# Performance work log

Measured on AMD Instinct MI355X. Metric: run time of the kernel, lower is better.

The kernel has to match this reference:

```python
import jax, jax.numpy as jnp
import numpy as np

N, NT, NX, H, M, DH, DIN = 16, 128, 128, 64, 12, 128, 128


def _spectral_conv(h, w1, w2, m):
    # h: [B,C,Ht,Wt]; w1,w2: complex [C,C,m,m]
    B, C, Ht, Wt = h.shape
    hft = jnp.fft.rfft2(h)  # [B,C,Ht,Wt//2+1] complex
    top = jnp.einsum('bixy,ioxy->boxy', hft[:, :, :m, :m], w1)
    bot = jnp.einsum('bixy,ioxy->boxy', hft[:, :, -m:, :m], w2)
    out_ft = jnp.zeros((B, w1.shape[1], Ht, Wt // 2 + 1), dtype=hft.dtype)
    out_ft = out_ft.at[:, :, :m, :m].set(top).at[:, :, -m:, :m].set(bot)
    return jnp.fft.irfft2(out_ft, s=(Ht, Wt))


def setup_inputs() -> dict:
    key = jax.random.key(0)
    ks = jax.random.split(key, 16)
    scale = 1.0 / (H * H)
    inp = {
        't': jax.random.uniform(ks[0], (NT,), jnp.float32),
        'x': jax.random.uniform(ks[1], (NX,), jnp.float32),
        'u0': jax.random.normal(ks[2], (N, DIN), jnp.float32),
        'fc0_w': jax.random.normal(ks[3], (H, DIN + 2), jnp.float32) / np.sqrt(DIN + 2),
        'fc0_b': jnp.zeros((H,), jnp.float32),
        'sc_w1_re': scale * jax.random.uniform(ks[4], (4, H, H, M, M), jnp.float32),
        'sc_w1_im': scale * jax.random.uniform(ks[5], (4, H, H, M, M), jnp.float32),
        'sc_w2_re': scale * jax.random.uniform(ks[6], (4, H, H, M, M), jnp.float32),
        'sc_w2_im': scale * jax.random.uniform(ks[7], (4, H, H, M, M), jnp.float32),
        'w_conv': jax.random.normal(ks[8], (4, H, H), jnp.float32) / np.sqrt(H),
        'b_conv': jnp.zeros((4, H), jnp.float32),
        'fc1_w': jax.random.normal(ks[9], (DH, H), jnp.float32) / np.sqrt(H),
        'fc1_b': jnp.zeros((DH,), jnp.float32),
        'fc2_w': jax.random.normal(ks[10], (1, DH), jnp.float32) / np.sqrt(DH),
        'fc2_b': jnp.zeros((1,), jnp.float32),
    }
    return inp


def reference(t, x, u0, fc0_w, fc0_b, sc_w1_re, sc_w1_im, sc_w2_re, sc_w2_im,
              w_conv, b_conv, fc1_w, fc1_b, fc2_w, fc2_b):
    nt, nx = t.shape[0], x.shape[0]
    n, din = u0.shape
    gelu = lambda v: jax.nn.gelu(v, approximate=False)  # torch F.gelu default (erf)
    # grid features, column order (x, t, u0) per torch hstack([query, aug_u0])
    xg = jnp.broadcast_to(x[None, None, :, None], (n, nt, nx, 1))
    tg = jnp.broadcast_to(t[None, :, None, None], (n, nt, nx, 1))
    ug = jnp.broadcast_to(u0[:, None, None, :], (n, nt, nx, din))
    h = jnp.concatenate([xg, tg, ug], axis=-1) @ fc0_w.T + fc0_b  # [N,Nt,Nx,H]
    h = jnp.transpose(h, (0, 3, 1, 2))  # [N,H,Nt,Nx]
    m = sc_w1_re.shape[-1]
    for i in range(4):
        w1 = sc_w1_re[i] + 1j * sc_w1_im[i]
        w2 = sc_w2_re[i] + 1j * sc_w2_im[i]
        x1 = _spectral_conv(h, w1, w2, m)
        x2 = jnp.einsum('bchw,oc->bohw', h, w_conv[i]) + b_conv[i][None, :, None, None]
        h = x1 + x2
        if i < 3:
            h = gelu(h)
    h = jnp.transpose(h, (0, 2, 3, 1))  # [N,Nt,Nx,H]
    h = gelu(h @ fc1_w.T + fc1_b)
    out = (h @ fc2_w.T + fc2_b)[..., 0]  # squeeze -> [N,Nt,Nx]
    return out
```

## Files before the change

kernel.cpp:

```cpp
#include <hip/hip_runtime.h>
#include <math.h>


typedef __attribute__((ext_vector_type(8))) short short8;
typedef __attribute__((ext_vector_type(4))) float f32x4;

__device__ inline unsigned short bf16rn(float v) {
    unsigned int b = __float_as_uint(v);
    return (unsigned short)((b + 0x7FFFu + ((b >> 16) & 1u)) >> 16);
}
__device__ inline void split2(float v, unsigned short& h, unsigned short& l) {
    h = bf16rn(v);
    float hf = __uint_as_float((unsigned int)h << 16);
    l = bf16rn(v - hf);
}
__device__ inline short8 ld8(const unsigned short* p) {
    return *reinterpret_cast<const short8*>(p);
}
__device__ inline float gelu_erf(float v) {
    return 0.5f * v * (1.0f + erff(v * 0.70710678118654752f));
}
#define MFMA3(accv, aH, aL, bH, bL) \
    accv = __builtin_amdgcn_mfma_f32_16x16x32_bf16(aH, bH, accv, 0, 0, 0); \
    accv = __builtin_amdgcn_mfma_f32_16x16x32_bf16(aH, bL, accv, 0, 0, 0); \
    accv = __builtin_amdgcn_mfma_f32_16x16x32_bf16(aL, bH, accv, 0, 0, 0);

#define STEPC 0.049087385212340519350f

__global__ __launch_bounds__(256) void k_tables2(unsigned short* TfH, unsigned short* TfL,
                                                 unsigned short* TiXH, unsigned short* TiXL,
                                                 unsigned short* TDH, unsigned short* TDL,
                                                 unsigned short* TIH, unsigned short* TIL) {
    int tid = threadIdx.x;
    unsigned short h, l;
    for (int i = tid; i < 32 * 128; i += 256) {
        int row = i >> 7, x = i & 127;
        float v = 0.f;
        if (row < 24) {
            int kx = row >> 1;
            float th = ((kx * x) & 127) * STEPC;
            v = (row & 1) ? -sinf(th) : cosf(th);
        }
        split2(v, h, l); TfH[i] = h; TfL[i] = l;
    }
    for (int i = tid; i < 128 * 32; i += 256) {
        int x = i >> 5, col = i & 31;
        float v = 0.f;
        if (col < 24) {
            int kx = col >> 1;
            float th = ((kx * x) & 127) * STEPC;
            float w = (kx == 0 ? 1.0f : 2.0f) / 16384.0f;
            v = (col & 1) ? -w * sinf(th) : w * cosf(th);
        }
        split2(v, h, l); TiXH[i] = h; TiXL[i] = l;
    }
    for (int i = tid; i < 48 * 256; i += 256) {
        int row = i >> 8, k = i & 255;
        int kt = row >> 1;
        int f = (kt < 12) ? kt : (kt + 104);
        int t = k & 127;
        float th = ((f * t) & 127) * STEPC;
        float c = cosf(th), s = sinf(th);
        float v;
        if (k < 128) v = (row & 1) ? -s : c;
        else         v = (row & 1) ?  c : s;
        split2(v, h, l); TDH[i] = h; TDL[i] = l;
    }
    for (int i = tid; i < 128 * 64; i += 256) {
        int t = i >> 6, col = i & 63;
        float v = 0.f;
        if (col < 48) {
            int kt = col >> 1;
            int f = (kt < 12) ? kt : (kt + 104);
            float th = ((f * t) & 127) * STEPC;
            v = (col & 1) ? -sinf(th) : cosf(th);
        }
        split2(v, h, l); TIH[i] = h; TIL[i] = l;
    }
}

__global__ void k_spec(const float* __restrict__ xs, const float* __restrict__ ts,
                       float2* __restrict__ Sx, float2* __restrict__ St) {
    int tid = threadIdx.x;
    if (tid < 12) {
        float re = 0.f, im = 0.f;
        for (int x = 0; x < 128; ++x) {
            float th = ((tid * x) & 127) * STEPC;
            re += xs[x] * cosf(th); im -= xs[x] * sinf(th);
        }
        Sx[tid] = make_float2(re, im);
    } else if (tid >= 32 && tid < 56) {
        int kt = tid - 32;
        int f = (kt < 12) ? kt : (kt + 104);
        float re = 0.f, im = 0.f;
        for (int t = 0; t < 128; ++t) {
            float th = ((f * t) & 127) * STEPC;
            re += ts[t] * cosf(th); im -= ts[t] * sinf(th);
        }
        St[kt] = make_float2(re, im);
    }
}

__global__ __launch_bounds__(256) void k_wprep(const float* __restrict__ wconv, const float* __restrict__ fc1w,
                                               unsigned short* WH, unsigned short* WL,
                                               unsigned short* F1H, unsigned short* F1L) {
    int i = blockIdx.x * 256 + threadIdx.x;
    if (i < 16384) split2(wconv[i], WH[i], WL[i]);
    if (i < 8192)  split2(fc1w[i], F1H[i], F1L[i]);
}

__global__ void k_u(const float* __restrict__ u0, const float* __restrict__ w,
                    const float* __restrict__ bias, float* __restrict__ U) {
    int b = blockIdx.x, c = threadIdx.x;
    float acc = bias[c];
    const float* wr = w + c * 130 + 2;
    const float* ur = u0 + b * 128;
    for (int d = 0; d < 128; ++d) acc += ur[d] * wr[d];
    U[b * 64 + c] = acc;
}

__global__ __launch_bounds__(256) void k_fc0t(const float* __restrict__ xs, const float* __restrict__ ts,
                                              const float* __restrict__ fc0_w, const float* __restrict__ U,
                                              unsigned short* __restrict__ hTH, unsigned short* __restrict__ hTL) {
    __shared__ float w0c[64], basec[64];
    int bid = blockIdx.x, tid = threadIdx.x;
    int t = bid & 127, b = bid >> 7;
    if (tid < 64) {
        w0c[tid] = fc0_w[tid * 130];
        basec[tid] = ts[t] * fc0_w[tid * 130 + 1] + U[b * 64 + tid];
    }
    __syncthreads();
    int x = tid >> 1, c0 = (tid & 1) * 32;
    float xv = xs[x];
    unsigned int ph[16], pl[16];
#pragma unroll
    for (int j = 0; j < 32; j += 2) {
        unsigned short h0, l0, h1, l1;
        split2(xv * w0c[c0 + j] + basec[c0 + j], h0, l0);
        split2(xv * w0c[c0 + j + 1] + basec[c0 + j + 1], h1, l1);
        ph[j >> 1] = (unsigned)h0 | ((unsigned)h1 << 16);
        pl[j >> 1] = (unsigned)l0 | ((unsigned)l1 << 16);
    }
    size_t rb = ((size_t)((b * 128 + t) * 128 + x)) * 64 + c0;
    uint4* dh = reinterpret_cast<uint4*>(&hTH[rb]);
    uint4* dl = reinterpret_cast<uint4*>(&hTL[rb]);
#pragma unroll
    for (int q = 0; q < 4; ++q) {
        dh[q] = make_uint4(ph[4 * q], ph[4 * q + 1], ph[4 * q + 2], ph[4 * q + 3]);
        dl[q] = make_uint4(pl[4 * q], pl[4 * q + 1], pl[4 * q + 2], pl[4 * q + 3]);
    }
}

__global__ __launch_bounds__(256) void k_hm0(const float* __restrict__ fc0_w, const float* __restrict__ U,
                                             const float2* __restrict__ Sx, const float2* __restrict__ St,
                                             float2* __restrict__ Hm) {
    __shared__ float w0s[64], w1s[64];
    int mode = blockIdx.x, tid = threadIdx.x;
    int kt = mode / 12, kx = mode - kt * 12;
    if (tid < 64) { w0s[tid] = fc0_w[tid * 130]; w1s[tid] = fc0_w[tid * 130 + 1]; }
    __syncthreads();
    float2 sx = Sx[kx], st = St[kt];
    for (int i = tid; i < 1024; i += 256) {
        int b = i >> 6, c = i & 63;
        float re = 0.f, im = 0.f;
        if (kt == 0) { re += 128.f * w0s[c] * sx.x; im += 128.f * w0s[c] * sx.y; }
        if (kx == 0) { re += 128.f * w1s[c] * st.x; im += 128.f * w1s[c] * st.y; }
        if (kt == 0 && kx == 0) re += 16384.f * U[b * 64 + c];
        Hm[((size_t)mode * 16 + b) * 64 + c] = make_float2(re, im);
    }
}

__global__ __launch_bounds__(256) void k_wt(const float* __restrict__ w1re, const float* __restrict__ w1im,
                                            const float* __restrict__ w2re, const float* __restrict__ w2im,
                                            float2* __restrict__ Wt) {
    __shared__ float ldsre[32 * 145];
    __shared__ float ldsim[32 * 145];
    int bid = blockIdx.x, tid = threadIdx.x;
    int c = bid & 63, tbl = (bid >> 6) & 1, l = bid >> 7;
    const float* re = (tbl ? w2re : w1re) + (size_t)((l * 64 + c) * 64) * 144;
    const float* im = (tbl ? w2im : w1im) + (size_t)((l * 64 + c) * 64) * 144;
    int moff = tbl * 144;
    for (int half = 0; half < 2; ++half) {
        __syncthreads();
        for (int i = tid; i < 32 * 144; i += 256) {
            int o = i / 144, m = i - o * 144;
            ldsre[o * 145 + m] = re[(half * 32 + o) * 144 + m];
            ldsim[o * 145 + m] = im[(half * 32 + o) * 144 + m];
        }
        __syncthreads();
        for (int i = tid; i < 32 * 144; i += 256) {
            int mode = i >> 5, o = i & 31;
            Wt[((size_t)(l * 288 + moff + mode) * 64 + c) * 64 + half * 32 + o] =
                make_float2(ldsre[o * 145 + mode], ldsim[o * 145 + mode]);
        }
    }
}

__global__ __launch_bounds__(256) void k_dftt2(const unsigned short* __restrict__ A2H, const unsigned short* __restrict__ A2L,
                                               const unsigned short* __restrict__ TDH, const unsigned short* __restrict__ TDL,
                                               float2* __restrict__ Hm) {
    int bid = blockIdx.x, tid = threadIdx.x;
    int b = bid / 12, kx = bid - b * 12;
    int w = tid >> 6, lane = tid & 63, ln = lane & 15, lg = lane >> 4;
    f32x4 acc[3];
#pragma unroll
    for (int m = 0; m < 3; ++m) acc[m] = (f32x4){0.f, 0.f, 0.f, 0.f};
    size_t reb = (size_t)(b * 24 + 2 * kx) * 64 * 128;
    size_t imb = (size_t)(b * 24 + 2 * kx + 1) * 64 * 128;
    int c = w * 16 + ln;
#pragma unroll
    for (int ks = 0; ks < 8; ++ks) {
        int k = ks * 32 + lg * 8;
        size_t boff = (ks < 4) ? (reb + (size_t)c * 128 + k) : (imb + (size_t)c * 128 + (k - 128));
        short8 bH = ld8(A2H + boff);
        short8 bL = ld8(A2L + boff);
#pragma unroll
        for (int m = 0; m < 3; ++m) {
            int aoff = (m * 16 + ln) * 256 + ks * 32 + lg * 8;
            short8 aH = ld8(TDH + aoff);
            short8 aL = ld8(TDL + aoff);
            MFMA3(acc[m], aH, aL, bH, bL);
        }
    }
    float* Hf = (float*)Hm;
#pragma unroll
    for (int m = 0; m < 3; ++m)
#pragma unroll
        for (int r = 0; r < 4; ++r) {
            int row = m * 16 + lg * 4 + r;
            int kt = row >> 1, p = row & 1;
            int mode = kt * 12 + kx;
            Hf[(((size_t)mode * 16 + b) * 64 + c) * 2 + p] = acc[m][r];
        }
}

__global__ __launch_bounds__(256) void k_mix(const float2* __restrict__ Hm, const float2* __restrict__ WtL,
                                             float2* __restrict__ Om) {
    __shared__ float2 hl[8 * 64];
    int bid = blockIdx.x, tid = threadIdx.x;
    int mode = bid >> 1, bh = bid & 1;
    const float2* hsrc = Hm + ((size_t)mode * 16 + bh * 8) * 64;
    for (int i = tid; i < 512; i += 256) hl[i] = hsrc[i];
    __syncthreads();
    int o = tid & 63, bg = tid >> 6;
    const float2* wp = WtL + (size_t)mode * 4096 + o;
    const float2* h0 = hl + (bg * 2) * 64;
    const float2* h1 = hl + (bg * 2 + 1) * 64;
    float a0r = 0.f, a0i = 0.f, a1r = 0.f, a1i = 0.f;
#pragma unroll 4
    for (int c = 0; c < 64; ++c) {
        float2 wv = wp[c * 64];
        float2 a0 = h0[c], a1 = h1[c];
        a0r += a0.x * wv.x - a0.y * wv.y;
        a0i += a0.x * wv.y + a0.y * wv.x;
        a1r += a1.x * wv.x - a1.y * wv.y;
        a1i += a1.x * wv.y + a1.y * wv.x;
    }
    int b0 = bh * 8 + bg * 2;
    Om[((size_t)(b0)*64 + o) * 288 + mode]       = make_float2(a0r, a0i);
    Om[((size_t)(b0 + 1) * 64 + o) * 288 + mode] = make_float2(a1r, a1i);
}

__global__ __launch_bounds__(256) void k_mix_raw(const float2* __restrict__ Hm,
                                                 const float* __restrict__ w1re, const float* __restrict__ w1im,
                                                 const float* __restrict__ w2re, const float* __restrict__ w2im,
                                                 float2* __restrict__ Om) {
    __shared__ float2 hl[8 * 64];
    int bid = blockIdx.x, tid = threadIdx.x;
    int mode = bid >> 1, bh = bid & 1;
    const float2* hsrc = Hm + ((size_t)mode * 16 + bh * 8) * 64;
    for (int i = tid; i < 512; i += 256) hl[i] = hsrc[i];
    __syncthreads();
    int kti = mode / 12, kx = mode - kti * 12;
    const float* re; const float* im; int ktw;
    if (kti < 12) { re = w1re; im = w1im; ktw = kti; }
    else          { re = w2re; im = w2im; ktw = kti - 12; }
    int off = ktw * 12 + kx;
    int o = tid & 63, bg = tid >> 6;
    const float2* h0 = hl + (bg * 2) * 64;
    const float2* h1 = hl + (bg * 2 + 1) * 64;
    float a0r = 0.f, a0i = 0.f, a1r = 0.f, a1i = 0.f;
    for (int c = 0; c < 64; ++c) {
        size_t widx = (size_t)(c * 64 + o) * 144 + off;
        float wr = re[widx], wi = im[widx];
        float2 a0 = h0[c], a1 = h1[c];
        a0r += a0.x * wr - a0.y * wi;
        a0i += a0.x * wi + a0.y * wr;
        a1r += a1.x * wr - a1.y * wi;
        a1i += a1.x * wi + a1.y * wr;
    }
    int b0 = bh * 8 + bg * 2;
    Om[((size_t)(b0)*64 + o) * 288 + mode]       = make_float2(a0r, a0i);
    Om[((size_t)(b0 + 1) * 64 + o) * 288 + mode] = make_float2(a1r, a1i);
}

__global__ __launch_bounds__(256) void k_idftt2(const float2* __restrict__ Om,
                                                const unsigned short* __restrict__ TIH, const unsigned short* __restrict__ TIL,
                                                unsigned short* __restrict__ BvH, unsigned short* __restrict__ BvL) {
    __shared__ unsigned short OmH[32][72], OmL[32][72];
    int bo = blockIdx.x, tid = threadIdx.x;
    unsigned int* zh = (unsigned int*)&OmH[0][0];
    unsigned int* zl = (unsigned int*)&OmL[0][0];
    for (int i = tid; i < 1152; i += 256) { zh[i] = 0u; zl[i] = 0u; }
    __syncthreads();
    const float2* src = Om + (size_t)bo * 288;
    for (int i = tid; i < 288; i += 256) {
        int kt = i / 12, kx = i - kt * 12;
        float2 o = src[i];
        unsigned short h, l;
        split2(o.x, h, l);  OmH[2 * kx][2 * kt] = h;     OmL[2 * kx][2 * kt] = l;
        split2(o.y, h, l);  OmH[2 * kx][2 * kt + 1] = h; OmL[2 * kx][2 * kt + 1] = l;
                            OmH[2 * kx + 1][2 * kt] = h; OmL[2 * kx + 1][2 * kt] = l;
        split2(-o.x, h, l); OmH[2 * kx + 1][2 * kt + 1] = h; OmL[2 * kx + 1][2 * kt + 1] = l;
    }
    __syncthreads();
    int w = tid >> 6, lane = tid & 63, ln = lane & 15, lg = lane >> 4;
    f32x4 acc[2][2];
#pragma unroll
    for (int mi = 0; mi < 2; ++mi)
#pragma unroll
        for (int nt = 0; nt < 2; ++nt) acc[mi][nt] = (f32x4){0.f, 0.f, 0.f, 0.f};
#pragma unroll
    for (int ks = 0; ks < 2; ++ks) {
        short8 bH[2], bL[2];
#pragma unroll
        for (int nt = 0; nt < 2; ++nt) {
            int boff = (nt * 16 + ln) * 72 + ks * 32 + lg * 8;
            bH[nt] = ld8(&OmH[0][0] + boff);
            bL[nt] = ld8(&OmL[0][0] + boff);
        }
#pragma unroll
        for (int mi = 0; mi < 2; ++mi) {
            int mt = w * 2 + mi;
            int aoff = (mt * 16 + ln) * 64 + ks * 32 + lg * 8;
            short8 aH = ld8(TIH + aoff);
            short8 aL = ld8(TIL + aoff);
#pragma unroll
            for (int nt = 0; nt < 2; ++nt) { MFMA3(acc[mi][nt], aH, aL, bH[nt], bL[nt]); }
        }
    }
#pragma unroll
    for (int mi = 0; mi < 2; ++mi)
#pragma unroll
        for (int nt = 0; nt < 2; ++nt)
#pragma unroll
            for (int r = 0; r < 4; ++r) {
                int trow = (w * 2 + mi) * 16 + lg * 4 + r;
                int col = nt * 16 + ln;
                unsigned short h, l;
                split2(acc[mi][nt][r], h, l);
                size_t p = ((size_t)bo * 128 + trow) * 32 + col;
                BvH[p] = h; BvL[p] = l;
            }
}

template <int DOGELU, int FUSE>
__global__ __launch_bounds__(256) void k_conv3(unsigned short* __restrict__ hTH, unsigned short* __restrict__ hTL,
                                               const unsigned short* __restrict__ WH, const unsigned short* __restrict__ WL,
                                               const unsigned short* __restrict__ BvH, const unsigned short* __restrict__ BvL,
                                               const unsigned short* __restrict__ TiXH, const unsigned short* __restrict__ TiXL,
                                               const unsigned short* __restrict__ TfH, const unsigned short* __restrict__ TfL,
                                               unsigned short* __restrict__ A2H, unsigned short* __restrict__ A2L,
                                               const float* __restrict__ bconv) {
    __shared__ float hsf[64][132];
    int bid = blockIdx.x, tid = threadIdx.x;
    int t = bid & 127, b = bid >> 7;
    int w = tid >> 6, lane = tid & 63, ln = lane & 15, lg = lane >> 4;
    size_t btbase = (size_t)(b * 128 + t) * 128 * 64;
    f32x4 acc[8];
#pragma unroll
    for (int nx = 0; nx < 8; ++nx) acc[nx] = (f32x4){0.f, 0.f, 0.f, 0.f};
#pragma unroll
    for (int kt = 0; kt < 2; ++kt) {
        int aoff = (w * 16 + ln) * 64 + kt * 32 + lg * 8;
        short8 aH = ld8(WH + aoff);
        short8 aL = ld8(WL + aoff);
#pragma unroll
        for (int nx = 0; nx < 8; ++nx) {
            size_t boff = btbase + (size_t)(nx * 16 + ln) * 64 + kt * 32 + lg * 8;
            short8 bH = ld8(hTH + boff);
            short8 bL = ld8(hTL + boff);
            MFMA3(acc[nx], aH, aL, bH, bL);
        }
    }
    {
        size_t aoff = ((size_t)(b * 64 + w * 16 + ln) * 128 + t) * 32 + lg * 8;
        short8 aH = ld8(BvH + aoff);
        short8 aL = ld8(BvL + aoff);
#pragma unroll
        for (int nx = 0; nx < 8; ++nx) {
            int boff = (nx * 16 + ln) * 32 + lg * 8;
            short8 bH = ld8(TiXH + boff);
            short8 bL = ld8(TiXL + boff);
            MFMA3(acc[nx], aH, aL, bH, bL);
        }
    }
    __syncthreads();
    int o0 = w * 16 + lg * 4;
    float bc0 = bconv[o0], bc1 = bconv[o0 + 1], bc2 = bconv[o0 + 2], bc3 = bconv[o0 + 3];
#pragma unroll
    for (int nx = 0; nx < 8; ++nx) {
        int x = nx * 16 + ln;
        float v0 = acc[nx][0] + bc0;
        float v1 = acc[nx][1] + bc1;
        float v2 = acc[nx][2] + bc2;
        float v3 = acc[nx][3] + bc3;
        if (DOGELU) { v0 = gelu_erf(v0); v1 = gelu_erf(v1); v2 = gelu_erf(v2); v3 = gelu_erf(v3); }
        unsigned short hh[4], ll[4];
        split2(v0, hh[0], ll[0]); split2(v1, hh[1], ll[1]);
        split2(v2, hh[2], ll[2]); split2(v3, hh[3], ll[3]);
        size_t trow = btbase + (size_t)x * 64 + o0;
        *reinterpret_cast<uint2*>(&hTH[trow]) =
            make_uint2((unsigned)hh[0] | ((unsigned)hh[1] << 16), (unsigned)hh[2] | ((unsigned)hh[3] << 16));
        *reinterpret_cast<uint2*>(&hTL[trow]) =
            make_uint2((unsigned)ll[0] | ((unsigned)ll[1] << 16), (unsigned)ll[2] | ((unsigned)ll[3] << 16));
        if (FUSE) {
            hsf[o0 + 0][x] = v0; hsf[o0 + 1][x] = v1;
            hsf[o0 + 2][x] = v2; hsf[o0 + 3][x] = v3;
        }
    }
    if (FUSE) {
        __syncthreads();
        int mw = w & 1, ng = (w >> 1) * 2;
        f32x4 acc2[2];
        acc2[0] = (f32x4){0.f, 0.f, 0.f, 0.f};
        acc2[1] = (f32x4){0.f, 0.f, 0.f, 0.f};
#pragma unroll
        for (int kt = 0; kt < 4; ++kt) {
            int aoff = (mw * 16 + ln) * 128 + kt * 32 + lg * 8;
            short8 aH = ld8(TfH + aoff);
            short8 aL = ld8(TfL + aoff);
#pragma unroll
            for (int j = 0; j < 2; ++j) {
                int c = (ng + j) * 16 + ln;
                float4 f0 = *reinterpret_cast<const float4*>(&hsf[c][kt * 32 + lg * 8]);
                float4 f1 = *reinterpret_cast<const float4*>(&hsf[c][kt * 32 + lg * 8 + 4]);
                short8 bH, bL;
                unsigned short h, l;
                split2(f0.x, h, l); bH[0] = (short)h; bL[0] = (short)l;
                split2(f0.y, h, l); bH[1] = (short)h; bL[1] = (short)l;
                split2(f0.z, h, l); bH[2] = (short)h; bL[2] = (short)l;
                split2(f0.w, h, l); bH[3] = (short)h; bL[3] = (short)l;
                split2(f1.x, h, l); bH[4] = (short)h; bL[4] = (short)l;
                split2(f1.y, h, l); bH[5] = (short)h; bL[5] = (short)l;
                split2(f1.z, h, l); bH[6] = (short)h; bL[6] = (short)l;
                split2(f1.w, h, l); bH[7] = (short)h; bL[7] = (short)l;
                MFMA3(acc2[j], aH, aL, bH, bL);
            }
        }
#pragma unroll
        for (int j = 0; j < 2; ++j) {
            int c = (ng + j) * 16 + ln;
#pragma unroll
            for (int r = 0; r < 4; ++r) {
                int col = mw * 16 + lg * 4 + r;
                if (col < 24) {
                    unsigned short h, l;
                    split2(acc2[j][r], h, l);
                    size_t addr = ((size_t)(b * 24 + col) * 64 + c) * 128 + t;
                    A2H[addr] = h; A2L[addr] = l;
                }
            }
        }
    }
}

__global__ __launch_bounds__(256) void k_head2(const unsigned short* __restrict__ hTH, const unsigned short* __restrict__ hTL,
                                               const unsigned short* __restrict__ F1H, const unsigned short* __restrict__ F1L,
                                               const float* __restrict__ b1, const float* __restrict__ w2,
                                               const float* __restrict__ b2, float* __restrict__ out) {
    __shared__ float red[16][66];
    int bid = blockIdx.x, tid = threadIdx.x;
    int xh = bid & 1, t = (bid >> 1) & 127, b = bid >> 8;
    int w = tid >> 6, lane = tid & 63, ln = lane & 15, lg = lane >> 4;
    f32x4 acc[2][4];
#pragma unroll
    for (int s = 0; s < 2; ++s)
#pragma unroll
        for (int nx = 0; nx < 4; ++nx) acc[s][nx] = (f32x4){0.f, 0.f, 0.f, 0.f};
    size_t btbase = ((size_t)(b * 128 + t) * 128 + xh * 64) * 64;
#pragma unroll
    for (int kt = 0; kt < 2; ++kt) {
        short8 bH[4], bL[4];
#pragma unroll
        for (int nx = 0; nx < 4; ++nx) {
            size_t boff = btbase + (size_t)(nx * 16 + ln) * 64 + kt * 32 + lg * 8;
            bH[nx] = ld8(hTH + boff);
            bL[nx] = ld8(hTL + boff);
        }
#pragma unroll
        for (int s = 0; s < 2; ++s) {
            int aoff = ((w * 2 + s) * 16 + ln) * 64 + kt * 32 + lg * 8;
            short8 aH = ld8(F1H + aoff);
            short8 aL = ld8(F1L + aoff);
#pragma unroll
            for (int nx = 0; nx < 4; ++nx) { MFMA3(acc[s][nx], aH, aL, bH[nx], bL[nx]); }
        }
    }
    float p[4] = {0.f, 0.f, 0.f, 0.f};
#pragma unroll
    for (int s = 0; s < 2; ++s)
#pragma unroll
        for (int r = 0; r < 4; ++r) {
            int d = (w * 2 + s) * 16 + lg * 4 + r;
            float bb = b1[d], wk = w2[d];
#pragma unroll
            for (int nx = 0; nx < 4; ++nx) {
                float v = acc[s][nx][r] + bb;
                p[nx] += gelu_erf(v) * wk;
            }
        }
#pragma unroll
    for (int nx = 0; nx < 4; ++nx) red[w * 4 + lg][nx * 16 + ln] = p[nx];
    __syncthreads();
    if (tid < 64) {
        float s = 0.f;
#pragma unroll
        for (int g = 0; g < 16; ++g) s += red[g][tid];
        out[((size_t)b * 128 + t) * 128 + xh * 64 + tid] = s + b2[0];
    }
}

extern "C" void kernel_launch(void* const* d_in, const int* in_sizes, int n_in,
                              void* d_out, int out_size, void* d_ws, size_t ws_size,
                              hipStream_t stream) {
    const float* ts    = (const float*)d_in[0];
    const float* xs    = (const float*)d_in[1];
    const float* u0    = (const float*)d_in[2];
    const float* fc0_w = (const float*)d_in[3];
    const float* fc0_b = (const float*)d_in[4];
    const float* w1re  = (const float*)d_in[5];
    const float* w1im  = (const float*)d_in[6];
    const float* w2re  = (const float*)d_in[7];
    const float* w2im  = (const float*)d_in[8];
    const float* wconv = (const float*)d_in[9];
    const float* bconv = (const float*)d_in[10];
    const float* fc1w  = (const float*)d_in[11];
    const float* fc1b  = (const float*)d_in[12];
    const float* fc2w  = (const float*)d_in[13];
    const float* fc2b  = (const float*)d_in[14];
    float* out = (float*)d_out;

    char* ws = (char*)d_ws;
    size_t off = 0;
    auto alloc = [&](size_t bytes) -> char* {
        char* p = ws + off;
        off = (off + bytes + 255) & ~(size_t)255;
        return p;
    };
    unsigned short* hTH = (unsigned short*)alloc(33554432);
    unsigned short* hTL = (unsigned short*)alloc(33554432);
    unsigned short* A2H = (unsigned short*)alloc(6291456);
    unsigned short* A2L = (unsigned short*)alloc(6291456);
    float2* Hm = (float2*)alloc(2359296);
    float2* Om = (float2*)alloc(2359296);
    unsigned short* BvH = (unsigned short*)alloc(8388608);
    unsigned short* BvL = (unsigned short*)alloc(8388608);
    float* U   = (float*)alloc(4096);
    float2* Sx = (float2*)alloc(256);
    float2* St = (float2*)alloc(256);
    unsigned short* TfH  = (unsigned short*)alloc(8192);
    unsigned short* TfL  = (unsigned short*)alloc(8192);
    unsigned short* TiXH = (unsigned short*)alloc(8192);
    unsigned short* TiXL = (unsigned short*)alloc(8192);
    unsigned short* TDH  = (unsigned short*)alloc(24576);
    unsigned short* TDL  = (unsigned short*)alloc(24576);
    unsigned short* TIH  = (unsigned short*)alloc(16384);
    unsigned short* TIL  = (unsigned short*)alloc(16384);
    unsigned short* WH   = (unsigned short*)alloc(32768);
    unsigned short* WL   = (unsigned short*)alloc(32768);
    unsigned short* F1H  = (unsigned short*)alloc(16384);
    unsigned short* F1L  = (unsigned short*)alloc(16384);
    size_t base_need = off;
    if (ws_size < base_need) return;
    float2* Wt = (float2*)alloc(37748736);
    bool use_wt = (ws_size >= off);

    k_tables2<<<1, 256, 0, stream>>>(TfH, TfL, TiXH, TiXL, TDH, TDL, TIH, TIL);
    k_spec<<<1, 64, 0, stream>>>(xs, ts, Sx, St);
    k_u<<<16, 64, 0, stream>>>(u0, fc0_w, fc0_b, U);
    k_wprep<<<64, 256, 0, stream>>>(wconv, fc1w, WH, WL, F1H, F1L);
    k_fc0t<<<2048, 256, 0, stream>>>(xs, ts, fc0_w, U, hTH, hTL);
    k_hm0<<<288, 256, 0, stream>>>(fc0_w, U, Sx, St, Hm);
    if (use_wt)
        k_wt<<<512, 256, 0, stream>>>(w1re, w1im, w2re, w2im, Wt);

    for (int l = 0; l < 4; ++l) {
        if (l > 0)
            k_dftt2<<<192, 256, 0, stream>>>(A2H, A2L, TDH, TDL, Hm);
        if (use_wt)
            k_mix<<<576, 256, 0, stream>>>(Hm, Wt + (size_t)l * 288 * 4096, Om);
        else
            k_mix_raw<<<576, 256, 0, stream>>>(Hm, w1re + (size_t)l * 589824, w1im + (size_t)l * 589824,
                                               w2re + (size_t)l * 589824, w2im + (size_t)l * 589824, Om);
        k_idftt2<<<1024, 256, 0, stream>>>(Om, TIH, TIL, BvH, BvL);
        if (l < 3)
            k_conv3<1, 1><<<2048, 256, 0, stream>>>(hTH, hTL, WH + l * 4096, WL + l * 4096,
                                                    BvH, BvL, TiXH, TiXL, TfH, TfL, A2H, A2L, bconv + l * 64);
        else
            k_conv3<0, 0><<<2048, 256, 0, stream>>>(hTH, hTL, WH + l * 4096, WL + l * 4096,
                                                    BvH, BvL, TiXH, TiXL, TfH, TfL, A2H, A2L, bconv + l * 64);
    }
    k_head2<<<4096, 256, 0, stream>>>(hTH, hTL, F1H, F1L, fc1b, fc2w, fc2b, out);
}
```

Baseline: 724.6 us.

## Fuse fc0 lifting into layer-0 conv, fuse last conv with head, relayout A2

Removes the k_fc0t kernel, which materialised the lifted hidden state, by noting that layer 0's pointwise conv of an affine function of (x, t, U) is itself affine. Precomputed W·fc0 columns and W·U+bias are applied in the layer-0 epilogue, so the first hT read and MFMA are skipped. The final conv layer is fused with the fc1/gelu/fc2 head through shared memory, avoiding a full hT write and re-read. The A2 intermediate is also changed to a t-major, channel-contiguous layout written with vectorised stores through LDS, and k_dftt2 transposes it in LDS. The cost is more LDS traffic and synchronisation, and higher register pressure in the fused head kernel.

Result: faster. 610.7 us (-15.7%).

```diff
diff --git a/kernel.cpp b/kernel.cpp
--- a/kernel.cpp
+++ b/kernel.cpp
@@ -54,16 +54,17 @@
         }
         split2(v, h, l); TiXH[i] = h; TiXL[i] = l;
     }
-    for (int i = tid; i < 48 * 256; i += 256) {
-        int row = i >> 8, k = i & 255;
+    for (int i = tid; i < 2 * 48 * 128; i += 256) {
+        int q = i >> 12;
+        int rem = i & 6143;
+        int row = rem >> 7, t = rem & 127;
         int kt = row >> 1;
         int f = (kt < 12) ? kt : (kt + 104);
-        int t = k & 127;
         float th = ((f * t) & 127) * STEPC;
         float c = cosf(th), s = sinf(th);
         float v;
-        if (k < 128) v = (row & 1) ? -s : c;
-        else         v = (row & 1) ?  c : s;
+        if (q == 0) v = (row & 1) ? -s : c;
+        else        v = (row & 1) ?  c : s;
         split2(v, h, l); TDH[i] = h; TDL[i] = l;
     }
     for (int i = tid; i < 128 * 64; i += 256) {
@@ -101,14 +102,6 @@
     }
 }
 
-__global__ __launch_bounds__(256) void k_wprep(const float* __restrict__ wconv, const float* __restrict__ fc1w,
-                                               unsigned short* WH, unsigned short* WL,
-                                               unsigned short* F1H, unsigned short* F1L) {
-    int i = blockIdx.x * 256 + threadIdx.x;
-    if (i < 16384) split2(wconv[i], WH[i], WL[i]);
-    if (i < 8192)  split2(fc1w[i], F1H[i], F1L[i]);
-}
-
 __global__ void k_u(const float* __restrict__ u0, const float* __restrict__ w,
                     const float* __restrict__ bias, float* __restrict__ U) {
     int b = blockIdx.x, c = threadIdx.x;
@@ -119,35 +112,30 @@
     U[b * 64 + c] = acc;
 }
 
-__global__ __launch_bounds__(256) void k_fc0t(const float* __restrict__ xs, const float* __restrict__ ts,
-                                              const float* __restrict__ fc0_w, const float* __restrict__ U,
-                                              unsigned short* __restrict__ hTH, unsigned short* __restrict__ hTL) {
-    __shared__ float w0c[64], basec[64];
-    int bid = blockIdx.x, tid = threadIdx.x;
-    int t = bid & 127, b = bid >> 7;
-    if (tid < 64) {
-        w0c[tid] = fc0_w[tid * 130];
-        basec[tid] = ts[t] * fc0_w[tid * 130 + 1] + U[b * 64 + tid];
-    }
-    __syncthreads();
-    int x = tid >> 1, c0 = (tid & 1) * 32;
-    float xv = xs[x];
-    unsigned int ph[16], pl[16];
-#pragma unroll
-    for (int j = 0; j < 32; j += 2) {
-        unsigned short h0, l0, h1, l1;
-        split2(xv * w0c[c0 + j] + basec[c0 + j], h0, l0);
-        split2(xv * w0c[c0 + j + 1] + basec[c0 + j + 1], h1, l1);
-        ph[j >> 1] = (unsigned)h0 | ((unsigned)h1 << 16);
-        pl[j >> 1] = (unsigned)l0 | ((unsigned)l1 << 16);
-    }
-    size_t rb = ((size_t)((b * 128 + t) * 128 + x)) * 64 + c0;
-    uint4* dh = reinterpret_cast<uint4*>(&hTH[rb]);
-    uint4* dl = reinterpret_cast<uint4*>(&hTL[rb]);
-#pragma unroll
-    for (int q = 0; q < 4; ++q) {
-        dh[q] = make_uint4(ph[4 * q], ph[4 * q + 1], ph[4 * q + 2], ph[4 * q + 3]);
-        dl[q] = make_uint4(pl[4 * q], pl[4 * q + 1], pl[4 * q + 2], pl[4 * q + 3]);
+__global__ __launch_bounds__(256) void k_wprep(const float* __restrict__ wconv, const float* __restrict__ fc1w,
+                                               unsigned short* WH, unsigned short* WL,
+                                               unsigned short* F1H, unsigned short* F1L) {
+    int i = blockIdx.x * 256 + threadIdx.x;
+    if (i < 16384) split2(wconv[i], WH[i], WL[i]);
+    if (i < 8192)  split2(fc1w[i], F1H[i], F1L[i]);
+}
+
+__global__ void k_cw(const float* __restrict__ wconv, const float* __restrict__ bconv,
+                     const float* __restrict__ fc0_w, const float* __restrict__ U,
+                     float* __restrict__ Ww0, float* __restrict__ Ww1, float* __restrict__ WU) {
+    int b = blockIdx.x, o = threadIdx.x;
+    const float* wr = wconv + o * 64;
+    float au = bconv[o];
+    const float* ur = U + b * 64;
+    for (int c = 0; c < 64; ++c) au += wr[c] * ur[c];
+    WU[b * 64 + o] = au;
+    if (b == 0) {
+        float a0 = 0.f, a1 = 0.f;
+        for (int c = 0; c < 64; ++c) {
+            a0 += wr[c] * fc0_w[c * 130];
+            a1 += wr[c] * fc0_w[c * 130 + 1];
+        }
+        Ww0[o] = a0; Ww1[o] = a1;
     }
 }
 
@@ -199,38 +187,54 @@
 __global__ __launch_bounds__(256) void k_dftt2(const unsigned short* __restrict__ A2H, const unsigned short* __restrict__ A2L,
                                                const unsigned short* __restrict__ TDH, const unsigned short* __restrict__ TDL,
                                                float2* __restrict__ Hm) {
+    __shared__ unsigned short sH[64][136], sL[64][136];
     int bid = blockIdx.x, tid = threadIdx.x;
     int b = bid / 12, kx = bid - b * 12;
     int w = tid >> 6, lane = tid & 63, ln = lane & 15, lg = lane >> 4;
     f32x4 acc[3];
 #pragma unroll
     for (int m = 0; m < 3; ++m) acc[m] = (f32x4){0.f, 0.f, 0.f, 0.f};
-    size_t reb = (size_t)(b * 24 + 2 * kx) * 64 * 128;
-    size_t imb = (size_t)(b * 24 + 2 * kx + 1) * 64 * 128;
+#pragma unroll
+    for (int q = 0; q < 2; ++q) {
+        if (q) __syncthreads();
+        int col = 2 * kx + q;
+        const unsigned short* srcH = A2H + (size_t)(b * 24 + col) * 128 * 64;
+        const unsigned short* srcL = A2L + (size_t)(b * 24 + col) * 128 * 64;
+        for (int i = tid; i < 1024; i += 256) {
+            int t = i >> 3, c0 = (i & 7) * 8;
+            uint4 vh = *reinterpret_cast<const uint4*>(srcH + t * 64 + c0);
+            uint4 vl = *reinterpret_cast<const uint4*>(srcL + t * 64 + c0);
+            const unsigned short* ph = (const unsigned short*)&vh;
+            const unsigned short* pl = (const unsigned short*)&vl;
+#pragma unroll
+            for (int j = 0; j < 8; ++j) {
+                sH[c0 + j][t] = ph[j];
+                sL[c0 + j][t] = pl[j];
+            }
+        }
+        __syncthreads();
+#pragma unroll
+        for (int ks = 0; ks < 4; ++ks) {
+            short8 bH = ld8(&sH[w * 16 + ln][ks * 32 + lg * 8]);
+            short8 bL = ld8(&sL[w * 16 + ln][ks * 32 + lg * 8]);
+#pragma unroll
+            for (int m = 0; m < 3; ++m) {
+                int aoff = (q * 48 + m * 16 + ln) * 128 + ks * 32 + lg * 8;
+                short8 aH = ld8(TDH + aoff);
+                short8 aL = ld8(TDL + aoff);
+                MFMA3(acc[m], aH, aL, bH, bL);
+            }
+        }
+    }
+    float* Hf = (float*)Hm;
     int c = w * 16 + ln;
-#pragma unroll
-    for (int ks = 0; ks < 8; ++ks) {
-        int k = ks * 32 + lg * 8;
-        size_t boff = (ks < 4) ? (reb + (size_t)c * 128 + k) : (imb + (size_t)c * 128 + (k - 128));
-        short8 bH = ld8(A2H + boff);
-        short8 bL = ld8(A2L + boff);
-#pragma unroll
-        for (int m = 0; m < 3; ++m) {
-            int aoff = (m * 16 + ln) * 256 + ks * 32 + lg * 8;
-            short8 aH = ld8(TDH + aoff);
-            short8 aL = ld8(TDL + aoff);
-            MFMA3(acc[m], aH, aL, bH, bL);
-        }
-    }
-    float* Hf = (float*)Hm;
 #pragma unroll
     for (int m = 0; m < 3; ++m)
 #pragma unroll
         for (int r = 0; r < 4; ++r) {
             int row = m * 16 + lg * 4 + r;
-            int kt = row >> 1, p = row & 1;
-            int mode = kt * 12 + kx;
-            Hf[(((size_t)mode * 16 + b) * 64 + c) * 2 + p] = acc[m][r];
+            int kt = row >> 1, pp = row & 1;
+            Hf[(((size_t)(kt * 12 + kx) * 16 + b) * 64 + c) * 2 + pp] = acc[m][r];
         }
 }
 
@@ -331,8 +335,7 @@
         }
 #pragma unroll
         for (int mi = 0; mi < 2; ++mi) {
-            int mt = w * 2 + mi;
-            int aoff = (mt * 16 + ln) * 64 + ks * 32 + lg * 8;
+            int aoff = ((w * 2 + mi) * 16 + ln) * 64 + ks * 32 + lg * 8;
             short8 aH = ld8(TIH + aoff);
             short8 aL = ld8(TIL + aoff);
 #pragma unroll
@@ -354,14 +357,17 @@
             }
 }
 
-template <int DOGELU, int FUSE>
-__global__ __launch_bounds__(256) void k_conv3(unsigned short* __restrict__ hTH, unsigned short* __restrict__ hTL,
-                                               const unsigned short* __restrict__ WH, const unsigned short* __restrict__ WL,
-                                               const unsigned short* __restrict__ BvH, const unsigned short* __restrict__ BvL,
-                                               const unsigned short* __restrict__ TiXH, const unsigned short* __restrict__ TiXL,
-                                               const unsigned short* __restrict__ TfH, const unsigned short* __restrict__ TfL,
-                                               unsigned short* __restrict__ A2H, unsigned short* __restrict__ A2L,
-                                               const float* __restrict__ bconv) {
+template <int AFFINE>
+__global__ __launch_bounds__(256) void k_conv_mid(unsigned short* __restrict__ hTH, unsigned short* __restrict__ hTL,
+                                                  const unsigned short* __restrict__ WH, const unsigned short* __restrict__ WL,
+                                                  const unsigned short* __restrict__ BvH, const unsigned short* __restrict__ BvL,
+                                                  const unsigned short* __restrict__ TiXH, const unsigned short* __restrict__ TiXL,
+                                                  const unsigned short* __restrict__ TfH, const unsigned short* __restrict__ TfL,
+                                                  unsigned short* __restrict__ A2H, unsigned short* __restrict__ A2L,
+                                                  const float* __restrict__ bconv,
+                                                  const float* __restrict__ xs, const float* __restrict__ ts,
+                                                  const float* __restrict__ Ww0, const float* __restrict__ Ww1,
+                                                  const float* __restrict__ WU) {
     __shared__ float hsf[64][132];
     int bid = blockIdx.x, tid = threadIdx.x;
     int t = bid & 127, b = bid >> 7;
@@ -370,17 +376,19 @@
     f32x4 acc[8];
 #pragma unroll
     for (int nx = 0; nx < 8; ++nx) acc[nx] = (f32x4){0.f, 0.f, 0.f, 0.f};
-#pragma unroll
-    for (int kt = 0; kt < 2; ++kt) {
-        int aoff = (w * 16 + ln) * 64 + kt * 32 + lg * 8;
-        short8 aH = ld8(WH + aoff);
-        short8 aL = ld8(WL + aoff);
-#pragma unroll
-        for (int nx = 0; nx < 8; ++nx) {
-            size_t boff = btbase + (size_t)(nx * 16 + ln) * 64 + kt * 32 + lg * 8;
-            short8 bH = ld8(hTH + boff);
-            short8 bL = ld8(hTL + boff);
-            MFMA3(acc[nx], aH, aL, bH, bL);
+    if (!AFFINE) {
+#pragma unroll
+        for (int kt = 0; kt < 2; ++kt) {
+            int aoff = (w * 16 + ln) * 64 + kt * 32 + lg * 8;
+            short8 aH = ld8(WH + aoff);
+            short8 aL = ld8(WL + aoff);
+#pragma unroll
+            for (int nx = 0; nx < 8; ++nx) {
+                size_t boff = btbase + (size_t)(nx * 16 + ln) * 64 + kt * 32 + lg * 8;
+                short8 bH = ld8(hTH + boff);
+                short8 bL = ld8(hTL + boff);
+                MFMA3(acc[nx], aH, aL, bH, bL);
+            }
         }
     }
     {
@@ -397,15 +405,28 @@
     }
     __syncthreads();
     int o0 = w * 16 + lg * 4;
-    float bc0 = bconv[o0], bc1 = bconv[o0 + 1], bc2 = bconv[o0 + 2], bc3 = bconv[o0 + 3];
+    float ad0, ad1, ad2, ad3, w00 = 0.f, w01 = 0.f, w02 = 0.f, w03 = 0.f;
+    float w10 = 0.f, w11 = 0.f, w12 = 0.f, w13 = 0.f, tsv = 0.f;
+    if (AFFINE) {
+        const float* wu = WU + b * 64 + o0;
+        ad0 = wu[0]; ad1 = wu[1]; ad2 = wu[2]; ad3 = wu[3];
+        w00 = Ww0[o0]; w01 = Ww0[o0 + 1]; w02 = Ww0[o0 + 2]; w03 = Ww0[o0 + 3];
+        tsv = ts[t];
+        w10 = Ww1[o0] * tsv; w11 = Ww1[o0 + 1] * tsv; w12 = Ww1[o0 + 2] * tsv; w13 = Ww1[o0 + 3] * tsv;
+        ad0 += w10; ad1 += w11; ad2 += w12; ad3 += w13;
+    } else {
+        ad0 = bconv[o0]; ad1 = bconv[o0 + 1]; ad2 = bconv[o0 + 2]; ad3 = bconv[o0 + 3];
+    }
 #pragma unroll
     for (int nx = 0; nx < 8; ++nx) {
         int x = nx * 16 + ln;
-        float v0 = acc[nx][0] + bc0;
-        float v1 = acc[nx][1] + bc1;
-        float v2 = acc[nx][2] + bc2;
-        float v3 = acc[nx][3] + bc3;
-        if (DOGELU) { v0 = gelu_erf(v0); v1 = gelu_erf(v1); v2 = gelu_erf(v2); v3 = gelu_erf(v3); }
+        float xv = AFFINE ? xs[x] : 0.f;
+        float v0 = acc[nx][0] + ad0;
+        float v1 = acc[nx][1] + ad1;
+        float v2 = acc[nx][2] + ad2;
+        float v3 = acc[nx][3] + ad3;
+        if (AFFINE) { v0 += xv * w00; v1 += xv * w01; v2 += xv * w02; v3 += xv * w03; }
+        v0 = gelu_erf(v0); v1 = gelu_erf(v1); v2 = gelu_erf(v2); v3 = gelu_erf(v3);
         unsigned short hh[4], ll[4];
         split2(v0, hh[0], ll[0]); split2(v1, hh[1], ll[1]);
         split2(v2, hh[2], ll[2]); split2(v3, hh[3], ll[3]);
@@ -414,110 +435,170 @@
             make_uint2((unsigned)hh[0] | ((unsigned)hh[1] << 16), (unsigned)hh[2] | ((unsigned)hh[3] << 16));
         *reinterpret_cast<uint2*>(&hTL[trow]) =
             make_uint2((unsigned)ll[0] | ((unsigned)ll[1] << 16), (unsigned)ll[2] | ((unsigned)ll[3] << 16));
-        if (FUSE) {
-            hsf[o0 + 0][x] = v0; hsf[o0 + 1][x] = v1;
-            hsf[o0 + 2][x] = v2; hsf[o0 + 3][x] = v3;
-        }
-    }
-    if (FUSE) {
-        __syncthreads();
-        int mw = w & 1, ng = (w >> 1) * 2;
-        f32x4 acc2[2];
-        acc2[0] = (f32x4){0.f, 0.f, 0.f, 0.f};
-        acc2[1] = (f32x4){0.f, 0.f, 0.f, 0.f};
-#pragma unroll
-        for (int kt = 0; kt < 4; ++kt) {
-            int aoff = (mw * 16 + ln) * 128 + kt * 32 + lg * 8;
-            short8 aH = ld8(TfH + aoff);
-            short8 aL = ld8(TfL + aoff);
-#pragma unroll
-            for (int j = 0; j < 2; ++j) {
-                int c = (ng + j) * 16 + ln;
-                float4 f0 = *reinterpret_cast<const float4*>(&hsf[c][kt * 32 + lg * 8]);
-                float4 f1 = *reinterpret_cast<const float4*>(&hsf[c][kt * 32 + lg * 8 + 4]);
-                short8 bH, bL;
-                unsigned short h, l;
-                split2(f0.x, h, l); bH[0] = (short)h; bL[0] = (short)l;
-                split2(f0.y, h, l); bH[1] = (short)h; bL[1] = (short)l;
-                split2(f0.z, h, l); bH[2] = (short)h; bL[2] = (short)l;
-                split2(f0.w, h, l); bH[3] = (short)h; bL[3] = (short)l;
-                split2(f1.x, h, l); bH[4] = (short)h; bL[4] = (short)l;
-                split2(f1.y, h, l); bH[5] = (short)h; bL[5] = (short)l;
-                split2(f1.z, h, l); bH[6] = (short)h; bL[6] = (short)l;
-                split2(f1.w, h, l); bH[7] = (short)h; bL[7] = (short)l;
-                MFMA3(acc2[j], aH, aL, bH, bL);
-            }
-        }
+        hsf[o0 + 0][x] = v0; hsf[o0 + 1][x] = v1;
+        hsf[o0 + 2][x] = v2; hsf[o0 + 3][x] = v3;
+    }
+    __syncthreads();
+    int mw = w & 1, ng = (w >> 1) * 2;
+    f32x4 acc2[2];
+    acc2[0] = (f32x4){0.f, 0.f, 0.f, 0.f};
+    acc2[1] = (f32x4){0.f, 0.f, 0.f, 0.f};
+#pragma unroll
+    for (int kt = 0; kt < 4; ++kt) {
+        int aoff = (mw * 16 + ln) * 128 + kt * 32 + lg * 8;
+        short8 aH = ld8(TfH + aoff);
+        short8 aL = ld8(TfL + aoff);
 #pragma unroll
         for (int j = 0; j < 2; ++j) {
             int c = (ng + j) * 16 + ln;
-#pragma unroll
-            for (int r = 0; r < 4; ++r) {
-                int col = mw * 16 + lg * 4 + r;
-                if (col < 24) {
-                    unsigned short h, l;
-                    split2(acc2[j][r], h, l);
-                    size_t addr = ((size_t)(b * 24 + col) * 64 + c) * 128 + t;
-                    A2H[addr] = h; A2L[addr] = l;
-                }
+            float4 f0 = *reinterpret_cast<const float4*>(&hsf[c][kt * 32 + lg * 8]);
+            float4 f1 = *reinterpret_cast<const float4*>(&hsf[c][kt * 32 + lg * 8 + 4]);
+            short8 bH, bL;
+            unsigned short h, l;
+            split2(f0.x, h, l); bH[0] = (short)h; bL[0] = (short)l;
+            split2(f0.y, h, l); bH[1] = (short)h; bL[1] = (short)l;
+            split2(f0.z, h, l); bH[2] = (short)h; bL[2] = (short)l;
+            split2(f0.w, h, l); bH[3] = (short)h; bL[3] = (short)l;
+            split2(f1.x, h, l); bH[4] = (short)h; bL[4] = (short)l;
+            split2(f1.y, h, l); bH[5] = (short)h; bL[5] = (short)l;
+            split2(f1.z, h, l); bH[6] = (short)h; bL[6] = (short)l;
+            split2(f1.w, h, l); bH[7] = (short)h; bL[7] = (short)l;
+            MFMA3(acc2[j], aH, aL, bH, bL);
+        }
+    }
+    __syncthreads();
+    float* A2s = &hsf[0][0];
+#pragma unroll
+    for (int j = 0; j < 2; ++j) {
+        int c = (ng + j) * 16 + ln;
+#pragma unroll
+        for (int r = 0; r < 4; ++r) {
+            int col = mw * 16 + lg * 4 + r;
+            A2s[col * 68 + c] = acc2[j][r];
+        }
+    }
+    __syncthreads();
+    {
+        int col = tid >> 3;
+        if (col < 24) {
+            int c0 = (tid & 7) * 8;
+            unsigned short hh[8], ll[8];
+#pragma unroll
+            for (int j = 0; j < 8; ++j) split2(A2s[col * 68 + c0 + j], hh[j], ll[j]);
+            size_t p = ((size_t)(b * 24 + col) * 128 + t) * 64 + c0;
+            *reinterpret_cast<uint4*>(&A2H[p]) = make_uint4(
+                (unsigned)hh[0] | ((unsigned)hh[1] << 16), (unsigned)hh[2] | ((unsigned)hh[3] << 16),
+                (unsigned)hh[4] | ((unsigned)hh[5] << 16), (unsigned)hh[6] | ((unsigned)hh[7] << 16));
+            *reinterpret_cast<uint4*>(&A2L[p]) = make_uint4(
+                (unsigned)ll[0] | ((unsigned)ll[1] << 16), (unsigned)ll[2] | ((unsigned)ll[3] << 16),
+                (unsigned)ll[4] | ((unsigned)ll[5] << 16), (unsigned)ll[6] | ((unsigned)ll[7] << 16));
+        }
+    }
+}
+
+__global__ __launch_bounds__(256) void k_conv_head(const unsigned short* __restrict__ hTH, const unsigned short* __restrict__ hTL,
+                                                   const unsigned short* __restrict__ WH, const unsigned short* __restrict__ WL,
+                                                   const unsigned short* __restrict__ BvH, const unsigned short* __restrict__ BvL,
+                                                   const unsigned short* __restrict__ TiXH, const unsigned short* __restrict__ TiXL,
+                                                   const float* __restrict__ bconv,
+                                                   const unsigned short* __restrict__ F1H, const unsigned short* __restrict__ F1L,
+                                                   const float* __restrict__ b1, const float* __restrict__ w2,
+                                                   const float* __restrict__ b2, float* __restrict__ out) {
+    __shared__ float hsf[64][132];
+    int bid = blockIdx.x, tid = threadIdx.x;
+    int t = bid & 127, b = bid >> 7;
+    int w = tid >> 6, lane = tid & 63, ln = lane & 15, lg = lane >> 4;
+    size_t btbase = (size_t)(b * 128 + t) * 128 * 64;
+    f32x4 acc[8];
+#pragma unroll
+    for (int nx = 0; nx < 8; ++nx) acc[nx] = (f32x4){0.f, 0.f, 0.f, 0.f};
+#pragma unroll
+    for (int kt = 0; kt < 2; ++kt) {
+        int aoff = (w * 16 + ln) * 64 + kt * 32 + lg * 8;
+        short8 aH = ld8(WH + aoff);
+        short8 aL = ld8(WL + aoff);
+#pragma unroll
+        for (int nx = 0; nx < 8; ++nx) {
+            size_t boff = btbase + (size_t)(nx * 16 + ln) * 64 + kt * 32 + lg * 8;
+            short8 bH = ld8(hTH + boff);
+            short8 bL = ld8(hTL + boff);
+            MFMA3(acc[nx], aH, aL, bH, bL);
+        }
+    }
+    {
+        size_t aoff = ((size_t)(b * 64 + w * 16 + ln) * 128 + t) * 32 + lg * 8;
+        short8 aH = ld8(BvH + aoff);
+        short8 aL = ld8(BvL + aoff);
+#pragma unroll
+        for (int nx = 0; nx < 8; ++nx) {
+            int boff = (nx * 16 + ln) * 32 + lg * 8;
+            short8 bH = ld8(TiXH + boff);
+            short8 bL = ld8(TiXL + boff);
+            MFMA3(acc[nx], aH, aL, bH, bL);
+        }
+    }
+    int o0 = w * 16 + lg * 4;
+    float bc0 = bconv[o0], bc1 = bconv[o0 + 1], bc2 = bconv[o0 + 2], bc3 = bconv[o0 + 3];
+#pragma unroll
+    for (int nx = 0; nx < 8; ++nx) {
+        int x = nx * 16 + ln;
+        hsf[o0 + 0][x] = acc[nx][0] + bc0;
+        hsf[o0 + 1][x] = acc[nx][1] + bc1;
+        hsf[o0 + 2][x] = acc[nx][2] + bc2;
+        hsf[o0 + 3][x] = acc[nx][3] + bc3;
+    }
+    __syncthreads();
+    f32x4 acc2[2][8];
+#pragma unroll
+    for (int mi = 0; mi < 2; ++mi)
+#pragma unroll
+        for (int nx = 0; nx < 8; ++nx) acc2[mi][nx] = (f32x4){0.f, 0.f, 0.f, 0.f};
+#pragma unroll
+    for (int kc = 0; kc < 2; ++kc) {
+        short8 bH[8], bL[8];
+#pragma unroll
+        for (int nx = 0; nx < 8; ++nx) {
+            int x = nx * 16 + ln;
+            int c0 = kc * 32 + lg * 8;
+            unsigned short h, l;
+#pragma unroll
+            for (int j = 0; j < 8; ++j) {
+                split2(hsf[c0 + j][x], h, l);
+                bH[nx][j] = (short)h; bL[nx][j] = (short)l;
             }
         }
-    }
-}
-
-__global__ __launch_bounds__(256) void k_head2(const unsigned short* __restrict__ hTH, const unsigned short* __restrict__ hTL,
-                                               const unsigned short* __restrict__ F1H, const unsigned short* __restrict__ F1L,
-                                               const float* __restrict__ b1, const float* __restrict__ w2,
-                                               const float* __restrict__ b2, float* __restrict__ out) {
-    __shared__ float red[16][66];
-    int bid = blockIdx.x, tid = threadIdx.x;
-    int xh = bid & 1, t = (bid >> 1) & 127, b = bid >> 8;
-    int w = tid >> 6, lane = tid & 63, ln = lane & 15, lg = lane >> 4;
-    f32x4 acc[2][4];
-#pragma unroll
-    for (int s = 0; s < 2; ++s)
-#pragma unroll
-        for (int nx = 0; nx < 4; ++nx) acc[s][nx] = (f32x4){0.f, 0.f, 0.f, 0.f};
-    size_t btbase = ((size_t)(b * 128 + t) * 128 + xh * 64) * 64;
-#pragma unroll
-    for (int kt = 0; kt < 2; ++kt) {
-        short8 bH[4], bL[4];
-#pragma unroll
-        for (int nx = 0; nx < 4; ++nx) {
-            size_t boff = btbase + (size_t)(nx * 16 + ln) * 64 + kt * 32 + lg * 8;
-            bH[nx] = ld8(hTH + boff);
-            bL[nx] = ld8(hTL + boff);
-        }
-#pragma unroll
-        for (int s = 0; s < 2; ++s) {
-            int aoff = ((w * 2 + s) * 16 + ln) * 64 + kt * 32 + lg * 8;
+#pragma unroll
+        for (int mi = 0; mi < 2; ++mi) {
+            int aoff = ((w * 2 + mi) * 16 + ln) * 64 + kc * 32 + lg * 8;
             short8 aH = ld8(F1H + aoff);
             short8 aL = ld8(F1L + aoff);
 #pragma unroll
-            for (int nx = 0; nx < 4; ++nx) { MFMA3(acc[s][nx], aH, aL, bH[nx], bL[nx]); }
-        }
-    }
-    float p[4] = {0.f, 0.f, 0.f, 0.f};
-#pragma unroll
-    for (int s = 0; s < 2; ++s)
+            for (int nx = 0; nx < 8; ++nx) { MFMA3(acc2[mi][nx], aH, aL, bH[nx], bL[nx]); }
+        }
+    }
+    float p[8] = {0.f, 0.f, 0.f, 0.f, 0.f, 0.f, 0.f, 0.f};
+#pragma unroll
+    for (int mi = 0; mi < 2; ++mi)
 #pragma unroll
         for (int r = 0; r < 4; ++r) {
-            int d = (w * 2 + s) * 16 + lg * 4 + r;
+            int d = (w * 2 + mi) * 16 + lg * 4 + r;
             float bb = b1[d], wk = w2[d];
 #pragma unroll
-            for (int nx = 0; nx < 4; ++nx) {
-                float v = acc[s][nx][r] + bb;
+            for (int nx = 0; nx < 8; ++nx) {
+                float v = acc2[mi][nx][r] + bb;
                 p[nx] += gelu_erf(v) * wk;
             }
         }
-#pragma unroll
-    for (int nx = 0; nx < 4; ++nx) red[w * 4 + lg][nx * 16 + ln] = p[nx];
-    __syncthreads();
-    if (tid < 64) {
+    __syncthreads();
+    float* red = &hsf[0][0];
+#pragma unroll
+    for (int nx = 0; nx < 8; ++nx) red[(w * 4 + lg) * 130 + nx * 16 + ln] = p[nx];
+    __syncthreads();
+    if (tid < 128) {
         float s = 0.f;
 #pragma unroll
-        for (int g = 0; g < 16; ++g) s += red[g][tid];
-        out[((size_t)b * 128 + t) * 128 + xh * 64 + tid] = s + b2[0];
+        for (int g = 0; g < 16; ++g) s += red[g * 130 + tid];
+        out[((size_t)b * 128 + t) * 128 + tid] = s + b2[0];
     }
 }
 
@@ -556,9 +637,12 @@
     float2* Om = (float2*)alloc(2359296);
     unsigned short* BvH = (unsigned short*)alloc(8388608);
     unsigned short* BvL = (unsigned short*)alloc(8388608);
-    float* U   = (float*)alloc(4096);
-    float2* Sx = (float2*)alloc(256);
-    float2* St = (float2*)alloc(256);
+    float* U    = (float*)alloc(4096);
+    float2* Sx  = (float2*)alloc(256);
+    float2* St  = (float2*)alloc(256);
+    float* Ww0  = (float*)alloc(256);
+    float* Ww1  = (float*)alloc(256);
+    float* WU   = (float*)alloc(4096);
     unsigned short* TfH  = (unsigned short*)alloc(8192);
     unsigned short* TfL  = (unsigned short*)alloc(8192);
     unsigned short* TiXH = (unsigned short*)alloc(8192);
@@ -580,7 +664,7 @@
     k_spec<<<1, 64, 0, stream>>>(xs, ts, Sx, St);
     k_u<<<16, 64, 0, stream>>>(u0, fc0_w, fc0_b, U);
     k_wprep<<<64, 256, 0, stream>>>(wconv, fc1w, WH, WL, F1H, F1L);
-    k_fc0t<<<2048, 256, 0, stream>>>(xs, ts, fc0_w, U, hTH, hTL);
+    k_cw<<<16, 64, 0, stream>>>(wconv, bconv, fc0_w, U, Ww0, Ww1, WU);
     k_hm0<<<288, 256, 0, stream>>>(fc0_w, U, Sx, St, Hm);
     if (use_wt)
         k_wt<<<512, 256, 0, stream>>>(w1re, w1im, w2re, w2im, Wt);
@@ -594,12 +678,16 @@
             k_mix_raw<<<576, 256, 0, stream>>>(Hm, w1re + (size_t)l * 589824, w1im + (size_t)l * 589824,
                                                w2re + (size_t)l * 589824, w2im + (size_t)l * 589824, Om);
         k_idftt2<<<1024, 256, 0, stream>>>(Om, TIH, TIL, BvH, BvL);
-        if (l < 3)
-            k_conv3<1, 1><<<2048, 256, 0, stream>>>(hTH, hTL, WH + l * 4096, WL + l * 4096,
-                                                    BvH, BvL, TiXH, TiXL, TfH, TfL, A2H, A2L, bconv + l * 64);
+        if (l == 0)
+            k_conv_mid<1><<<2048, 256, 0, stream>>>(hTH, hTL, WH, WL, BvH, BvL, TiXH, TiXL,
+                                                    TfH, TfL, A2H, A2L, bconv, xs, ts, Ww0, Ww1, WU);
+        else if (l < 3)
+            k_conv_mid<0><<<2048, 256, 0, stream>>>(hTH, hTL, WH + l * 4096, WL + l * 4096,
+                                                    BvH, BvL, TiXH, TiXL, TfH, TfL, A2H, A2L,
+                                                    bconv + l * 64, xs, ts, Ww0, Ww1, WU);
         else
-            k_conv3<0, 0><<<2048, 256, 0, stream>>>(hTH, hTL, WH + l * 4096, WL + l * 4096,
-                                                    BvH, BvL, TiXH, TiXL, TfH, TfL, A2H, A2L, bconv + l * 64);
-    }
-    k_head2<<<4096, 256, 0, stream>>>(hTH, hTL, F1H, F1L, fc1b, fc2w, fc2b, out);
-}
+            k_conv_head<<<2048, 256, 0, stream>>>(hTH, hTL, WH + 3 * 4096, WL + 3 * 4096,
+                                                  BvH, BvL, TiXH, TiXL, bconv + 3 * 64,
+                                                  F1H, F1L, fc1b, fc2w, fc2b, out);
+    }
+}
```
